# Performance work log

Hardware: AMD Instinct MI355X
Metric: run time of the kernel (lower is better)

Reference implementation:

```python
import jax, jax.numpy as jnp
import numpy as np

T, B = 128, 256      # seq_len, batch
D = 1024             # input_dim (embedding dim)
H = 1024             # hidden_dim
NQ = 8               # n_qubits
V = 32000            # vocab_size
TAGS = 1024          # tagset_size


def setup_inputs() -> dict:
    key = jax.random.key(0)
    ks = jax.random.split(key, 10)
    s = 0.05
    return {
        "sentence": jax.random.randint(ks[0], (T, B), 0, V),
        "emb": jax.random.normal(ks[1], (V, D), jnp.float32) * s,
        # gate order: forget, input, update, output (stacked on leading axis)
        "Wg": jax.random.normal(ks[2], (4, D + H, NQ), jnp.float32) * s,
        "bg": jax.random.normal(ks[3], (4, NQ), jnp.float32) * s,
        "theta": jax.random.normal(ks[4], (4, NQ), jnp.float32) * s,  # trainable RX angles
        "Wp": jax.random.normal(ks[5], (4, NQ, H), jnp.float32) * s,
        "bp": jax.random.normal(ks[6], (4, H), jnp.float32) * s,
        "W_tag": jax.random.normal(ks[7], (H, TAGS), jnp.float32) * s,
        "b_tag": jax.random.normal(ks[8], (TAGS,), jnp.float32) * s,
    }


def reference(sentence, emb, Wg, bg, theta, Wp, bp, W_tag, b_tag):
    embeds = emb[sentence]                      # (T, B, D)
    bsz = embeds.shape[1]
    hidden = Wp.shape[2]

    def step(carry, x):
        hx, cx = carry
        comb = jnp.concatenate([x, hx], axis=1)                       # (B, D+H)
        raw = jnp.einsum('bc,gcq->gbq', comb, Wg) + bg[:, None, :]    # (4, B, NQ)
        # QLayer: RX(x) then trainable RX(theta) per wire on |0>, measure Z
        # -> product state, <Z_i> = cos(raw_i + theta_i)  (exact)
        q = jnp.cos(raw + theta[:, None, :])                          # (4, B, NQ)
        proj = jnp.einsum('gbq,gqh->gbh', q, Wp) + bp[:, None, :]     # (4, B, H)
        f = jax.nn.sigmoid(proj[0])
        i = jax.nn.sigmoid(proj[1])
        g = jnp.tanh(proj[2])
        o = jax.nn.sigmoid(proj[3])
        cx = f * cx + i * g
        hx = o * jnp.tanh(cx)
        return (hx, cx), hx

    hx0 = jnp.zeros((bsz, hidden), embeds.dtype)
    cx0 = jnp.zeros((bsz, hidden), embeds.dtype)
    _, lstm_out = jax.lax.scan(step, (hx0, cx0), embeds)              # (T, B, H)
    tag_logits = lstm_out @ W_tag + b_tag                             # (T, B, TAGS)
    # torch applies log_softmax over dim=1 (the batch axis) -- faithful
    return jax.nn.log_softmax(tag_logits, axis=1)
```

## Files before the change

kernel.cpp:

```cpp
#include <hip/hip_runtime.h>
#include <hip/hip_bf16.h>
#include <stdint.h>

#define T_LEN 128
#define B_SZ  256
#define D_IN  1024
#define H_DIM 1024
#define NQ    8
#define VOCAB 32000
#define TAGS  1024

typedef __attribute__((ext_vector_type(8))) short short8;
typedef __attribute__((ext_vector_type(4))) float f32x4;

__device__ __forceinline__ unsigned short f2bf_bits(float x) {
    __hip_bfloat16 h = __float2bfloat16(x);
    unsigned short u; __builtin_memcpy(&u, &h, 2); return u;
}
__device__ __forceinline__ uint32_t pack_bf2(float a, float b) {
    return (uint32_t)f2bf_bits(a) | ((uint32_t)f2bf_bits(b) << 16);
}
__device__ __forceinline__ float sigmoid_f(float x) {
    return 1.f / (1.f + __expf(-x));
}
__device__ __forceinline__ float tanh_f(float x) {
    return 1.f - 2.f / (__expf(2.f * x) + 1.f);
}
__device__ __forceinline__ void gload_lds16(void* lds_base, const void* gptr) {
    __builtin_amdgcn_global_load_lds(
        (__attribute__((address_space(1))) const void*)gptr,
        (__attribute__((address_space(3))) void*)lds_base,
        16, 0, 0);
}

__global__ __launch_bounds__(256) void k_wt_transpose(const float* __restrict__ W,
                                                      __hip_bfloat16* __restrict__ WtT) {
    __shared__ float tile[32][33];
    const int kb = blockIdx.x * 32, nb = blockIdx.y * 32;
    const int r = threadIdx.x >> 5, c = threadIdx.x & 31;
#pragma unroll
    for (int i = 0; i < 4; ++i)
        tile[r + 8 * i][c] = W[(size_t)(kb + r + 8 * i) * TAGS + nb + c];
    __syncthreads();
#pragma unroll
    for (int i = 0; i < 4; ++i)
        WtT[(size_t)(nb + r + 8 * i) * H_DIM + kb + c] = __float2bfloat16(tile[c][r + 8 * i]);
}

#define GXB_ROWS 32
__global__ __launch_bounds__(256, 2) void k_gx(
    const int* __restrict__ sent, const float* __restrict__ emb,
    const float* __restrict__ Wg, const float* __restrict__ bg,
    const float* __restrict__ theta, float* __restrict__ gx)
{
    __shared__ float xs[2][1024];
    const int tid = threadIdx.x, lane = tid & 63, wv = tid >> 6;
    const int ol = lane & 7, s = lane >> 3;
    const int o = wv * 8 + ol;

    float wk[128];
#pragma unroll
    for (int k = 0; k < 32; ++k)
#pragma unroll
        for (int e = 0; e < 4; ++e) {
            const int c = (s + 8 * k) * 4 + e;
            wk[4 * k + e] = Wg[((size_t)wv * 2048 + c) * 8 + ol];
        }
    const float bt = bg[o] + theta[o];

    const int rbase = blockIdx.x * GXB_ROWS;
    const float4* emb4 = (const float4*)emb;
    float4 xn = emb4[(size_t)sent[rbase] * 256 + tid];
    *(float4*)&xs[0][4 * tid] = xn;
    __syncthreads();

    int cur = 0;
    for (int i8 = 0; i8 < GXB_ROWS / 8; ++i8) {
        float gacc[8];
#pragma unroll
        for (int ii = 0; ii < 8; ++ii) {
            const int i = i8 * 8 + ii;
            const bool havenext = (i + 1 < GXB_ROWS);
            if (havenext)
                xn = emb4[(size_t)sent[rbase + i + 1] * 256 + tid];

            const float4* x4 = (const float4*)xs[cur];
            float a0 = 0.f, a1 = 0.f, a2 = 0.f, a3 = 0.f;
#pragma unroll
            for (int k = 0; k < 32; ++k) {
                float4 v = x4[s + 8 * k];
                a0 = fmaf(wk[4 * k + 0], v.x, a0);
                a1 = fmaf(wk[4 * k + 1], v.y, a1);
                a2 = fmaf(wk[4 * k + 2], v.z, a2);
                a3 = fmaf(wk[4 * k + 3], v.w, a3);
            }
            float a = (a0 + a1) + (a2 + a3);
#pragma unroll
            for (int d = 8; d < 64; d <<= 1) a += __shfl_xor(a, d, 64);
            gacc[ii] = a + bt;

            if (havenext)
                *(float4*)&xs[cur ^ 1][4 * tid] = xn;
            __syncthreads();
            cur ^= 1;
        }
        if (lane < 8) {
#pragma unroll
            for (int ii = 0; ii < 8; ++ii)
                gx[(size_t)(rbase + i8 * 8 + ii) * 32 + wv * 8 + lane] = gacc[ii];
        }
    }
}

__global__ __launch_bounds__(512, 2) void k_qlstm(
    const float* __restrict__ gx, const float* __restrict__ Wg,
    const float* __restrict__ Wp, const float* __restrict__ bp,
    __hip_bfloat16* __restrict__ hb)
{
    __shared__ uint32_t hsb[512];
    __shared__ float red[8 * 32];
    __shared__ __attribute__((aligned(16))) float qs[32];
    __shared__ float gxl[T_LEN * 32];

    const int tid = threadIdx.x, lane = tid & 63, wv = tid >> 6;
    const int b = blockIdx.x;
    const int lg = lane >> 4;
    const int K0 = wv * 128;

    union { short8 s8; uint32_t u[4]; } wf[2][4];
#pragma unroll
    for (int ro = 0; ro < 2; ++ro) {
        const int o = ro * 16 + (lane & 15);
        const int g = o >> 3, q = o & 7;
#pragma unroll
        for (int kt = 0; kt < 4; ++kt) {
            const int k0 = K0 + kt * 32 + lg * 8;
#pragma unroll
            for (int p = 0; p < 4; ++p) {
                float e0 = Wg[((size_t)g * 2048 + 1024 + k0 + 2 * p) * 8 + q];
                float e1 = Wg[((size_t)g * 2048 + 1024 + k0 + 2 * p + 1) * 8 + q];
                wf[ro][kt].u[p] = pack_bf2(e0, e1);
            }
        }
    }
    float wpA[32], wpB[32];
#pragma unroll
    for (int j = 0; j < 32; ++j) {
        wpA[j] = Wp[(size_t)j * H_DIM + 2 * tid];
        wpB[j] = Wp[(size_t)j * H_DIM + 2 * tid + 1];
    }
    float bpA[4], bpB[4];
#pragma unroll
    for (int gg = 0; gg < 4; ++gg) {
        bpA[gg] = bp[gg * H_DIM + 2 * tid];
        bpB[gg] = bp[gg * H_DIM + 2 * tid + 1];
    }

    for (int i = tid; i < T_LEN * 32; i += 512)
        gxl[i] = gx[((size_t)(i >> 5) * B_SZ + b) * 32 + (i & 31)];

    hsb[tid] = 0u;
    float cx0 = 0.f, cx1 = 0.f;
    __syncthreads();

    uint32_t* hb32 = (uint32_t*)hb;
    const f32x4 zf = (f32x4){0.f, 0.f, 0.f, 0.f};

    for (int t8 = 0; t8 < T_LEN / 8; ++t8) {
        uint32_t hv8[8];
#pragma unroll
        for (int tt = 0; tt < 8; ++tt) {
            const int t = t8 * 8 + tt;

            f32x4 p0 = zf, p1 = zf;
#pragma unroll
            for (int kt = 0; kt < 4; ++kt) {
                short8 bf = *(const short8*)((const char*)hsb + 2 * K0 + 64 * kt + lg * 16);
                p0 = __builtin_amdgcn_mfma_f32_16x16x32_bf16(wf[0][kt].s8, bf, p0, 0, 0, 0);
                p1 = __builtin_amdgcn_mfma_f32_16x16x32_bf16(wf[1][kt].s8, bf, p1, 0, 0, 0);
            }
            if ((lane & 15) == 0) {
                *(f32x4*)&red[wv * 32 + 4 * lg] = p0;
                *(f32x4*)&red[wv * 32 + 16 + 4 * lg] = p1;
            }
            __syncthreads();

            if (tid < 32) {
                float r = gxl[t * 32 + tid];
#pragma unroll
                for (int w = 0; w < 8; ++w) r += red[w * 32 + tid];
                qs[tid] = __cosf(r);
            }
            __syncthreads();

            const float4* q4 = (const float4*)qs;
            float pjA[4], pjB[4];
#pragma unroll
            for (int gg = 0; gg < 4; ++gg) {
                float4 u = q4[2 * gg], v = q4[2 * gg + 1];
                pjA[gg] = bpA[gg]
                        + u.x * wpA[gg * 8 + 0] + u.y * wpA[gg * 8 + 1]
                        + u.z * wpA[gg * 8 + 2] + u.w * wpA[gg * 8 + 3]
                        + v.x * wpA[gg * 8 + 4] + v.y * wpA[gg * 8 + 5]
                        + v.z * wpA[gg * 8 + 6] + v.w * wpA[gg * 8 + 7];
                pjB[gg] = bpB[gg]
                        + u.x * wpB[gg * 8 + 0] + u.y * wpB[gg * 8 + 1]
                        + u.z * wpB[gg * 8 + 2] + u.w * wpB[gg * 8 + 3]
                        + v.x * wpB[gg * 8 + 4] + v.y * wpB[gg * 8 + 5]
                        + v.z * wpB[gg * 8 + 6] + v.w * wpB[gg * 8 + 7];
            }
            const float fA = sigmoid_f(pjA[0]), iA = sigmoid_f(pjA[1]);
            const float gA = tanh_f(pjA[2]),   oA = sigmoid_f(pjA[3]);
            const float fB = sigmoid_f(pjB[0]), iB = sigmoid_f(pjB[1]);
            const float gB = tanh_f(pjB[2]),   oB = sigmoid_f(pjB[3]);
            cx0 = fA * cx0 + iA * gA;
            cx1 = fB * cx1 + iB * gB;
            const float hv0 = oA * tanh_f(cx0);
            const float hv1 = oB * tanh_f(cx1);
            const uint32_t hvp = pack_bf2(hv0, hv1);
            hsb[tid] = hvp;
            hv8[tt] = hvp;
            __syncthreads();
        }
#pragma unroll
        for (int tt = 0; tt < 8; ++tt)
            hb32[((size_t)(t8 * 8 + tt) * B_SZ + b) * 512 + tid] = hv8[tt];
    }
}

__global__ __launch_bounds__(256) void k_tag_gemm(const __hip_bfloat16* __restrict__ Hb,
                                                  const __hip_bfloat16* __restrict__ WtT,
                                                  float* __restrict__ out)
{
    __shared__ short As[128 * 32];
    __shared__ short Bs[128 * 32];
    const int m0 = blockIdx.x * 128, n0 = blockIdx.y * 128;
    const int tid = threadIdx.x, lane = tid & 63, wid = tid >> 6;
    const int wm = (wid & 1) * 64, wn = (wid >> 1) * 64;
    const int mrow = lane & 15, quad = lane >> 4;

    const short* Hs = (const short*)Hb;
    const short* Ws = (const short*)WtT;

    f32x4 acc[4][4];
#pragma unroll
    for (int mi = 0; mi < 4; ++mi)
#pragma unroll
        for (int ni = 0; ni < 4; ++ni)
            acc[mi][ni] = (f32x4){0.f, 0.f, 0.f, 0.f};

    for (int kt = 0; kt < 32; ++kt) {
        const int k0 = kt * 32;
        __syncthreads();
#pragma unroll
        for (int ch = 0; ch < 2; ++ch) {
            const int chunk = wid + ch * 4;
            const int row = chunk * 16 + (lane >> 2);
            const int kc = (lane & 3) * 8;
            gload_lds16(&As[chunk * 512], &Hs[(size_t)(m0 + row) * H_DIM + k0 + kc]);
            gload_lds16(&Bs[chunk * 512], &Ws[(size_t)(n0 + row) * H_DIM + k0 + kc]);
        }
        __syncthreads();

        short8 afr[4], bfr[4];
#pragma unroll
        for (int mi = 0; mi < 4; ++mi)
            afr[mi] = *(const short8*)&As[(wm + mi * 16 + mrow) * 32 + quad * 8];
#pragma unroll
        for (int ni = 0; ni < 4; ++ni)
            bfr[ni] = *(const short8*)&Bs[(wn + ni * 16 + mrow) * 32 + quad * 8];
#pragma unroll
        for (int mi = 0; mi < 4; ++mi)
#pragma unroll
            for (int ni = 0; ni < 4; ++ni)
                acc[mi][ni] = __builtin_amdgcn_mfma_f32_16x16x32_bf16(
                    afr[mi], bfr[ni], acc[mi][ni], 0, 0, 0);
    }

#pragma unroll
    for (int mi = 0; mi < 4; ++mi)
#pragma unroll
        for (int ni = 0; ni < 4; ++ni)
#pragma unroll
            for (int r = 0; r < 4; ++r) {
                const int grow = m0 + wm + mi * 16 + quad * 4 + r;
                const int gcol = n0 + wn + ni * 16 + mrow;
                out[(size_t)grow * TAGS + gcol] = acc[mi][ni][r];
            }
}

#define LSM_COLS 32
__global__ __launch_bounds__(256) void k_logsoftmax(float* __restrict__ out) {
    __shared__ float tile[256 * LSM_COLS];
    __shared__ float lse[LSM_COLS];
    const int t = blockIdx.x, n0 = blockIdx.y * LSM_COLS;
    const int tid = threadIdx.x;
    float* base = out + (size_t)t * B_SZ * TAGS + n0;

    for (int i = tid; i < 256 * LSM_COLS; i += 256) {
        const int b = i >> 5, c = i & (LSM_COLS - 1);
        tile[i] = base[(size_t)b * TAGS + c];
    }
    __syncthreads();
    if (tid < LSM_COLS) {
        float m = -1e30f;
        for (int b = 0; b < 256; ++b) m = fmaxf(m, tile[b * LSM_COLS + tid]);
        float s = 0.f;
        for (int b = 0; b < 256; ++b) s += __expf(tile[b * LSM_COLS + tid] - m);
        lse[tid] = m + __logf(s);
    }
    __syncthreads();
    for (int i = tid; i < 256 * LSM_COLS; i += 256) {
        const int b = i >> 5, c = i & (LSM_COLS - 1);
        base[(size_t)b * TAGS + c] = tile[i] - lse[c];
    }
}

extern "C" void kernel_launch(void* const* d_in, const int* in_sizes, int n_in,
                              void* d_out, int out_size, void* d_ws, size_t ws_size,
                              hipStream_t stream) {
    (void)in_sizes; (void)n_in; (void)out_size; (void)ws_size;
    const int*   sent  = (const int*)d_in[0];
    const float* emb   = (const float*)d_in[1];
    const float* Wg    = (const float*)d_in[2];
    const float* bg    = (const float*)d_in[3];
    const float* theta = (const float*)d_in[4];
    const float* Wp    = (const float*)d_in[5];
    const float* bp    = (const float*)d_in[6];
    const float* Wt    = (const float*)d_in[7];
    float* out = (float*)d_out;

    __hip_bfloat16* hb  = (__hip_bfloat16*)d_ws;
    __hip_bfloat16* WtT = (__hip_bfloat16*)((char*)d_ws + (size_t)64 * 1024 * 1024);
    float* gx = (float*)d_out;

    k_wt_transpose<<<dim3(32, 32), 256, 0, stream>>>(Wt, WtT);
    k_gx<<<dim3((T_LEN * B_SZ) / GXB_ROWS), 256, 0, stream>>>(sent, emb, Wg, bg, theta, gx);
    k_qlstm<<<dim3(B_SZ), 512, 0, stream>>>(gx, Wg, Wp, bp, hb);
    k_tag_gemm<<<dim3(256, 8), 256, 0, stream>>>(hb, WtT, out);
    k_logsoftmax<<<dim3(T_LEN, TAGS / LSM_COLS), 256, 0, stream>>>(out);
}
```

Measured before the change: 628.3 us.

## Fuse batch-axis log-softmax into tag GEMM and shrink LSTM block to 256 threads

The tag GEMM now uses 256-row M tiles covering one full timestep's batch, so the log-softmax over the batch axis is computed in the GEMM epilogue. This removes the separate log-softmax kernel and its extra read and write of the output. The recurrent LSTM kernel moves from 512 to 256 threads per block. Each thread handles four hidden units, the cosine values are broadcast with shuffles instead of through shared memory, and one barrier per step is dropped. The trade-off is more registers per thread and longer MFMA chains per wave in the recurrence.

```diff
diff --git a/kernel.cpp b/kernel.cpp
--- a/kernel.cpp
+++ b/kernel.cpp
@@ -112,28 +112,28 @@
     }
 }
 
-__global__ __launch_bounds__(512, 2) void k_qlstm(
+__global__ __launch_bounds__(256, 1) void k_qlstm(
     const float* __restrict__ gx, const float* __restrict__ Wg,
     const float* __restrict__ Wp, const float* __restrict__ bp,
     __hip_bfloat16* __restrict__ hb)
 {
     __shared__ uint32_t hsb[512];
-    __shared__ float red[8 * 32];
-    __shared__ __attribute__((aligned(16))) float qs[32];
+    __shared__ float red[4 * 36];
     __shared__ float gxl[T_LEN * 32];
 
     const int tid = threadIdx.x, lane = tid & 63, wv = tid >> 6;
     const int b = blockIdx.x;
     const int lg = lane >> 4;
-    const int K0 = wv * 128;
-
-    union { short8 s8; uint32_t u[4]; } wf[2][4];
+    const int K0 = wv * 256;
+    const int ol = lane & 31;
+
+    union { short8 s8; uint32_t u[4]; } wf[2][8];
 #pragma unroll
     for (int ro = 0; ro < 2; ++ro) {
         const int o = ro * 16 + (lane & 15);
         const int g = o >> 3, q = o & 7;
 #pragma unroll
-        for (int kt = 0; kt < 4; ++kt) {
+        for (int kt = 0; kt < 8; ++kt) {
             const int k0 = K0 + kt * 32 + lg * 8;
 #pragma unroll
             for (int p = 0; p < 4; ++p) {
@@ -143,101 +143,103 @@
             }
         }
     }
-    float wpA[32], wpB[32];
-#pragma unroll
-    for (int j = 0; j < 32; ++j) {
-        wpA[j] = Wp[(size_t)j * H_DIM + 2 * tid];
-        wpB[j] = Wp[(size_t)j * H_DIM + 2 * tid + 1];
-    }
-    float bpA[4], bpB[4];
-#pragma unroll
-    for (int gg = 0; gg < 4; ++gg) {
-        bpA[gg] = bp[gg * H_DIM + 2 * tid];
-        bpB[gg] = bp[gg * H_DIM + 2 * tid + 1];
-    }
-
-    for (int i = tid; i < T_LEN * 32; i += 512)
+    float wpv[4][32], bpv[4][4];
+#pragma unroll
+    for (int hh = 0; hh < 4; ++hh) {
+#pragma unroll
+        for (int j = 0; j < 32; ++j)
+            wpv[hh][j] = Wp[(size_t)j * H_DIM + 4 * tid + hh];
+#pragma unroll
+        for (int gg = 0; gg < 4; ++gg)
+            bpv[hh][gg] = bp[gg * H_DIM + 4 * tid + hh];
+    }
+
+    for (int i = tid; i < T_LEN * 32; i += 256)
         gxl[i] = gx[((size_t)(i >> 5) * B_SZ + b) * 32 + (i & 31)];
 
-    hsb[tid] = 0u;
-    float cx0 = 0.f, cx1 = 0.f;
-    __syncthreads();
-
-    uint32_t* hb32 = (uint32_t*)hb;
+    *(uint2*)&hsb[2 * tid] = (uint2){0u, 0u};
+    float cx0 = 0.f, cx1 = 0.f, cx2 = 0.f, cx3 = 0.f;
+    __syncthreads();
+
     const f32x4 zf = (f32x4){0.f, 0.f, 0.f, 0.f};
 
     for (int t8 = 0; t8 < T_LEN / 8; ++t8) {
-        uint32_t hv8[8];
+        uint2 hv8[8];
 #pragma unroll
         for (int tt = 0; tt < 8; ++tt) {
             const int t = t8 * 8 + tt;
 
-            f32x4 p0 = zf, p1 = zf;
-#pragma unroll
-            for (int kt = 0; kt < 4; ++kt) {
-                short8 bf = *(const short8*)((const char*)hsb + 2 * K0 + 64 * kt + lg * 16);
-                p0 = __builtin_amdgcn_mfma_f32_16x16x32_bf16(wf[0][kt].s8, bf, p0, 0, 0, 0);
-                p1 = __builtin_amdgcn_mfma_f32_16x16x32_bf16(wf[1][kt].s8, bf, p1, 0, 0, 0);
-            }
+            f32x4 p0a = zf, p0b = zf, p1a = zf, p1b = zf;
+#pragma unroll
+            for (int kt = 0; kt < 8; kt += 2) {
+                short8 bfA = *(const short8*)((const char*)hsb + 2 * K0 + 64 * kt + lg * 16);
+                short8 bfB = *(const short8*)((const char*)hsb + 2 * K0 + 64 * (kt + 1) + lg * 16);
+                p0a = __builtin_amdgcn_mfma_f32_16x16x32_bf16(wf[0][kt].s8, bfA, p0a, 0, 0, 0);
+                p1a = __builtin_amdgcn_mfma_f32_16x16x32_bf16(wf[1][kt].s8, bfA, p1a, 0, 0, 0);
+                p0b = __builtin_amdgcn_mfma_f32_16x16x32_bf16(wf[0][kt + 1].s8, bfB, p0b, 0, 0, 0);
+                p1b = __builtin_amdgcn_mfma_f32_16x16x32_bf16(wf[1][kt + 1].s8, bfB, p1b, 0, 0, 0);
+            }
+            f32x4 p0 = p0a + p0b, p1 = p1a + p1b;
             if ((lane & 15) == 0) {
-                *(f32x4*)&red[wv * 32 + 4 * lg] = p0;
-                *(f32x4*)&red[wv * 32 + 16 + 4 * lg] = p1;
+                *(f32x4*)&red[wv * 36 + 4 * lg] = p0;
+                *(f32x4*)&red[wv * 36 + 16 + 4 * lg] = p1;
             }
             __syncthreads();
 
-            if (tid < 32) {
-                float r = gxl[t * 32 + tid];
-#pragma unroll
-                for (int w = 0; w < 8; ++w) r += red[w * 32 + tid];
-                qs[tid] = __cosf(r);
-            }
-            __syncthreads();
-
-            const float4* q4 = (const float4*)qs;
-            float pjA[4], pjB[4];
-#pragma unroll
-            for (int gg = 0; gg < 4; ++gg) {
-                float4 u = q4[2 * gg], v = q4[2 * gg + 1];
-                pjA[gg] = bpA[gg]
-                        + u.x * wpA[gg * 8 + 0] + u.y * wpA[gg * 8 + 1]
-                        + u.z * wpA[gg * 8 + 2] + u.w * wpA[gg * 8 + 3]
-                        + v.x * wpA[gg * 8 + 4] + v.y * wpA[gg * 8 + 5]
-                        + v.z * wpA[gg * 8 + 6] + v.w * wpA[gg * 8 + 7];
-                pjB[gg] = bpB[gg]
-                        + u.x * wpB[gg * 8 + 0] + u.y * wpB[gg * 8 + 1]
-                        + u.z * wpB[gg * 8 + 2] + u.w * wpB[gg * 8 + 3]
-                        + v.x * wpB[gg * 8 + 4] + v.y * wpB[gg * 8 + 5]
-                        + v.z * wpB[gg * 8 + 6] + v.w * wpB[gg * 8 + 7];
-            }
-            const float fA = sigmoid_f(pjA[0]), iA = sigmoid_f(pjA[1]);
-            const float gA = tanh_f(pjA[2]),   oA = sigmoid_f(pjA[3]);
-            const float fB = sigmoid_f(pjB[0]), iB = sigmoid_f(pjB[1]);
-            const float gB = tanh_f(pjB[2]),   oB = sigmoid_f(pjB[3]);
-            cx0 = fA * cx0 + iA * gA;
-            cx1 = fB * cx1 + iB * gB;
-            const float hv0 = oA * tanh_f(cx0);
-            const float hv1 = oB * tanh_f(cx1);
-            const uint32_t hvp = pack_bf2(hv0, hv1);
-            hsb[tid] = hvp;
+            float r = gxl[t * 32 + ol]
+                    + red[0 * 36 + ol] + red[1 * 36 + ol]
+                    + red[2 * 36 + ol] + red[3 * 36 + ol];
+            const float qv = __cosf(r);
+            float qa[32];
+#pragma unroll
+            for (int o = 0; o < 32; ++o) qa[o] = __shfl(qv, o, 64);
+
+            float hv[4];
+#pragma unroll
+            for (int hh = 0; hh < 4; ++hh) {
+                float pj[4];
+#pragma unroll
+                for (int gg = 0; gg < 4; ++gg) {
+                    float s = bpv[hh][gg];
+#pragma unroll
+                    for (int j = 0; j < 8; ++j)
+                        s = fmaf(qa[gg * 8 + j], wpv[hh][gg * 8 + j], s);
+                    pj[gg] = s;
+                }
+                const float f_ = sigmoid_f(pj[0]);
+                const float i_ = sigmoid_f(pj[1]);
+                const float g_ = tanh_f(pj[2]);
+                const float o_ = sigmoid_f(pj[3]);
+                float& cx = (hh == 0) ? cx0 : (hh == 1) ? cx1 : (hh == 2) ? cx2 : cx3;
+                cx = f_ * cx + i_ * g_;
+                hv[hh] = o_ * tanh_f(cx);
+            }
+            const uint2 hvp = (uint2){pack_bf2(hv[0], hv[1]), pack_bf2(hv[2], hv[3])};
+            *(uint2*)&hsb[2 * tid] = hvp;
             hv8[tt] = hvp;
             __syncthreads();
         }
 #pragma unroll
         for (int tt = 0; tt < 8; ++tt)
-            hb32[((size_t)(t8 * 8 + tt) * B_SZ + b) * 512 + tid] = hv8[tt];
-    }
-}
-
-__global__ __launch_bounds__(256) void k_tag_gemm(const __hip_bfloat16* __restrict__ Hb,
-                                                  const __hip_bfloat16* __restrict__ WtT,
-                                                  float* __restrict__ out)
+            ((uint2*)hb)[((size_t)(t8 * 8 + tt) * B_SZ + b) * 256 + tid] = hv8[tt];
+    }
+}
+
+__global__ __launch_bounds__(512) void k_tag_gemm_lsm(const __hip_bfloat16* __restrict__ Hb,
+                                                      const __hip_bfloat16* __restrict__ WtT,
+                                                      float* __restrict__ out)
 {
-    __shared__ short As[128 * 32];
+    __shared__ short As[256 * 32];
     __shared__ short Bs[128 * 32];
-    const int m0 = blockIdx.x * 128, n0 = blockIdx.y * 128;
+    __shared__ float wred[8][64];
+    __shared__ float wsum[8][64];
+
+    const int t = blockIdx.x, n0 = blockIdx.y * 128;
+    const int m0 = t * 256;
     const int tid = threadIdx.x, lane = tid & 63, wid = tid >> 6;
-    const int wm = (wid & 1) * 64, wn = (wid >> 1) * 64;
+    const int wm = (wid & 3) * 64, wn = (wid >> 2) * 64;
     const int mrow = lane & 15, quad = lane >> 4;
+    const int nh = wid >> 2, mw = wid & 3;
 
     const short* Hs = (const short*)Hb;
     const short* Ws = (const short*)WtT;
@@ -253,12 +255,17 @@
         const int k0 = kt * 32;
         __syncthreads();
 #pragma unroll
-        for (int ch = 0; ch < 2; ++ch) {
-            const int chunk = wid + ch * 4;
-            const int row = chunk * 16 + (lane >> 2);
+        for (int rd = 0; rd < 2; ++rd) {
+            const int c = wid + rd * 8;
+            const int row = c * 16 + (lane >> 2);
             const int kc = (lane & 3) * 8;
-            gload_lds16(&As[chunk * 512], &Hs[(size_t)(m0 + row) * H_DIM + k0 + kc]);
-            gload_lds16(&Bs[chunk * 512], &Ws[(size_t)(n0 + row) * H_DIM + k0 + kc]);
+            gload_lds16(&As[c * 512], &Hs[(size_t)(m0 + row) * H_DIM + k0 + kc]);
+        }
+        {
+            const int c = wid;
+            const int row = c * 16 + (lane >> 2);
+            const int kc = (lane & 3) * 8;
+            gload_lds16(&Bs[c * 512], &Ws[(size_t)(n0 + row) * H_DIM + k0 + kc]);
         }
         __syncthreads();
 
@@ -277,6 +284,56 @@
                     afr[mi], bfr[ni], acc[mi][ni], 0, 0, 0);
     }
 
+    float cmax[4];
+#pragma unroll
+    for (int ni = 0; ni < 4; ++ni) {
+        float m = -1e30f;
+#pragma unroll
+        for (int mi = 0; mi < 4; ++mi)
+#pragma unroll
+            for (int r = 0; r < 4; ++r) m = fmaxf(m, acc[mi][ni][r]);
+        m = fmaxf(m, __shfl_xor(m, 16, 64));
+        m = fmaxf(m, __shfl_xor(m, 32, 64));
+        cmax[ni] = m;
+    }
+    if (quad == 0) {
+#pragma unroll
+        for (int ni = 0; ni < 4; ++ni) wred[nh * 4 + mw][ni * 16 + mrow] = cmax[ni];
+    }
+    __syncthreads();
+#pragma unroll
+    for (int ni = 0; ni < 4; ++ni) {
+        float m = wred[nh * 4 + 0][ni * 16 + mrow];
+        m = fmaxf(m, wred[nh * 4 + 1][ni * 16 + mrow]);
+        m = fmaxf(m, wred[nh * 4 + 2][ni * 16 + mrow]);
+        m = fmaxf(m, wred[nh * 4 + 3][ni * 16 + mrow]);
+        cmax[ni] = m;
+    }
+    float lse[4];
+#pragma unroll
+    for (int ni = 0; ni < 4; ++ni) {
+        float s = 0.f;
+#pragma unroll
+        for (int mi = 0; mi < 4; ++mi)
+#pragma unroll
+            for (int r = 0; r < 4; ++r) s += __expf(acc[mi][ni][r] - cmax[ni]);
+        s += __shfl_xor(s, 16, 64);
+        s += __shfl_xor(s, 32, 64);
+        lse[ni] = s;
+    }
+    if (quad == 0) {
+#pragma unroll
+        for (int ni = 0; ni < 4; ++ni) wsum[nh * 4 + mw][ni * 16 + mrow] = lse[ni];
+    }
+    __syncthreads();
+#pragma unroll
+    for (int ni = 0; ni < 4; ++ni) {
+        const float s = wsum[nh * 4 + 0][ni * 16 + mrow]
+                      + wsum[nh * 4 + 1][ni * 16 + mrow]
+                      + wsum[nh * 4 + 2][ni * 16 + mrow]
+                      + wsum[nh * 4 + 3][ni * 16 + mrow];
+        lse[ni] = cmax[ni] + __logf(s);
+    }
 #pragma unroll
     for (int mi = 0; mi < 4; ++mi)
 #pragma unroll
@@ -285,35 +342,8 @@
             for (int r = 0; r < 4; ++r) {
                 const int grow = m0 + wm + mi * 16 + quad * 4 + r;
                 const int gcol = n0 + wn + ni * 16 + mrow;
-                out[(size_t)grow * TAGS + gcol] = acc[mi][ni][r];
-            }
-}
-
-#define LSM_COLS 32
-__global__ __launch_bounds__(256) void k_logsoftmax(float* __restrict__ out) {
-    __shared__ float tile[256 * LSM_COLS];
-    __shared__ float lse[LSM_COLS];
-    const int t = blockIdx.x, n0 = blockIdx.y * LSM_COLS;
-    const int tid = threadIdx.x;
-    float* base = out + (size_t)t * B_SZ * TAGS + n0;
-
-    for (int i = tid; i < 256 * LSM_COLS; i += 256) {
-        const int b = i >> 5, c = i & (LSM_COLS - 1);
-        tile[i] = base[(size_t)b * TAGS + c];
-    }
-    __syncthreads();
-    if (tid < LSM_COLS) {
-        float m = -1e30f;
-        for (int b = 0; b < 256; ++b) m = fmaxf(m, tile[b * LSM_COLS + tid]);
-        float s = 0.f;
-        for (int b = 0; b < 256; ++b) s += __expf(tile[b * LSM_COLS + tid] - m);
-        lse[tid] = m + __logf(s);
-    }
-    __syncthreads();
-    for (int i = tid; i < 256 * LSM_COLS; i += 256) {
-        const int b = i >> 5, c = i & (LSM_COLS - 1);
-        base[(size_t)b * TAGS + c] = tile[i] - lse[c];
-    }
+                out[(size_t)grow * TAGS + gcol] = acc[mi][ni][r] - lse[ni];
+            }
 }
 
 extern "C" void kernel_launch(void* const* d_in, const int* in_sizes, int n_in,
@@ -336,7 +366,6 @@
 
     k_wt_transpose<<<dim3(32, 32), 256, 0, stream>>>(Wt, WtT);
     k_gx<<<dim3((T_LEN * B_SZ) / GXB_ROWS), 256, 0, stream>>>(sent, emb, Wg, bg, theta, gx);
-    k_qlstm<<<dim3(B_SZ), 512, 0, stream>>>(gx, Wg, Wp, bp, hb);
-    k_tag_gemm<<<dim3(256, 8), 256, 0, stream>>>(hb, WtT, out);
-    k_logsoftmax<<<dim3(T_LEN, TAGS / LSM_COLS), 256, 0, stream>>>(out);
-}
+    k_qlstm<<<dim3(B_SZ), 256, 0, stream>>>(gx, Wg, Wp, bp, hb);
+    k_tag_gemm_lsm<<<dim3(T_LEN, TAGS / 128), 512, 0, stream>>>(hb, WtT, out);
+}
```

After: 574.3 us. 1.09x faster.
